# Optimization experiments

Measured on AMD Instinct MI355X. Metric: run time of the kernel, lower is better.

## Reference

```python
import jax, jax.numpy as jnp
import numpy as np

S = 14
L_COORD = 5.0
L_NOOBJ = 0.5


def setup_inputs() -> dict:
    key = jax.random.key(0)
    k1, k2, k3, k4 = jax.random.split(key, 4)
    N = 4096
    # positive uniforms so sqrt(w), sqrt(h) and IoU areas are well-defined (as in real YOLO outputs)
    pred_tensor = jax.random.uniform(k1, (N, S, S, 30), dtype=jnp.float32, minval=0.01, maxval=1.0)
    target_boxes = jax.random.uniform(k2, (N, S, S, 4), dtype=jnp.float32, minval=0.01, maxval=1.0)
    target_cls = jax.random.uniform(k3, (N, S, S, 20), dtype=jnp.float32)
    has_object_map = jax.random.bernoulli(k4, 0.15, (N, S, S))
    return {"pred_tensor": pred_tensor, "target_boxes": target_boxes,
            "target_cls": target_cls, "has_object_map": has_object_map}


def _xywh2xyxy(b):
    # b: (..., 4) as [cx, cy, w, h]; cx,cy are in grid units -> divide by S
    x, y, w, h = b[..., 0], b[..., 1], b[..., 2], b[..., 3]
    return jnp.stack([x / S - 0.5 * w, y / S - 0.5 * h,
                      x / S + 0.5 * w, y / S + 0.5 * h], axis=-1)


def _iou_pairwise(b1, b2):
    # elementwise IoU between matched boxes (diag of compute_iou), b: (..., 4) xyxy
    lt = jnp.maximum(b1[..., :2], b2[..., :2])
    rb = jnp.minimum(b1[..., 2:], b2[..., 2:])
    wh = jnp.maximum(rb - lt, 0.0)
    inter = wh[..., 0] * wh[..., 1]
    a1 = (b1[..., 2] - b1[..., 0]) * (b1[..., 3] - b1[..., 1])
    a2 = (b2[..., 2] - b2[..., 0]) * (b2[..., 3] - b2[..., 1])
    return inter / (a1 + a2 - inter)


def reference(pred_tensor, target_boxes, target_cls, has_object_map):
    N = pred_tensor.shape[0]
    obj = has_object_map.astype(pred_tensor.dtype)          # (N,S,S)
    noobj = 1.0 - obj

    box1 = pred_tensor[..., 0:5]
    box2 = pred_tensor[..., 5:10]
    pred_cls = pred_tensor[..., 10:]

    # class loss: masked sum-MSE over object cells
    cls_loss = jnp.sum(obj[..., None] * (pred_cls - target_cls) ** 2)

    # no-object loss: confidences of both predictors in non-object cells vs 0
    no_obj_loss = L_NOOBJ * jnp.sum(noobj * (box1[..., 4] ** 2 + box2[..., 4] ** 2))

    # best-of-B selection by IoU against target (elementwise, matched per cell)
    tgt_xyxy = _xywh2xyxy(target_boxes)
    iou1 = _iou_pairwise(_xywh2xyxy(box1[..., :4]), tgt_xyxy)
    iou2 = _iou_pairwise(_xywh2xyxy(box2[..., :4]), tgt_xyxy)
    take1 = iou1 > iou2
    best_iou = jnp.where(take1, iou1, iou2)                  # (N,S,S)
    best_box = jnp.where(take1[..., None], box1, box2)       # (N,S,S,5)

    xy_err = jnp.sum((best_box[..., :2] - target_boxes[..., :2]) ** 2, axis=-1)
    wh_err = jnp.sum((jnp.sqrt(best_box[..., 2:4]) - jnp.sqrt(target_boxes[..., 2:4])) ** 2, axis=-1)
    reg_loss = L_COORD * jnp.sum(obj * (xy_err + wh_err))

    # containing-object confidence loss; target IoU is detached
    contain_loss = jnp.sum(obj * (best_box[..., 4] - jax.lax.stop_gradient(best_iou)) ** 2)

    total = cls_loss + no_obj_loss + contain_loss + reg_loss
    # [total, reg, containing_obj, no_obj, cls], each averaged over batch
    return jnp.stack([total, reg_loss, contain_loss, no_obj_loss, cls_loss]) / N
```

## Files before the change

kernel.cpp:

```cpp
#include <hip/hip_runtime.h>


#define CELLS   802816
#define THREADS 256
#define NBLK    1024
#define NWAVES  (NBLK * 4)
#define CHUNK   32
#define CHUNKS  (CELLS / CHUNK)
#define L_COORD 5.0f
#define L_NOOBJ 0.5f

__global__ __launch_bounds__(THREADS, 4) void yolo_main(
    const float* __restrict__ pred,
    const float* __restrict__ tbox,
    const float* __restrict__ tcls,
    const int*   __restrict__ objmap,
    float4*      __restrict__ part)
{
    __shared__ float lds[4 * 960];
    __shared__ float red[4][4];

    const int tid  = threadIdx.x;
    const int wv   = tid >> 6;
    const int lane = tid & 63;
    float*  seg = &lds[wv * 960];
    float4* s4  = (float4*)seg;

    const int cc0 = lane / 5,   ch0 = (lane - cc0 * 5) * 4;
    const int i1  = lane + 64;
    const int cc1 = i1 / 5,     ch1 = (i1 - cc1 * 5) * 4;
    const int i2  = lane + 128;
    const int cc2 = (lane < 32) ? (i2 / 5) : 0;
    const int ch2 = (lane < 32) ? (i2 - cc2 * 5) * 4 : 0;
    const int bcell = lane >> 1;
    const int box   = lane & 1;
    const float invS = 1.0f / 14.0f;

    float acc_reg = 0.f, acc_cont = 0.f, acc_noobj = 0.f, acc_cls = 0.f;

    int c = blockIdx.x * 4 + wv;

    {
        const float4* p4 = (const float4*)pred + (size_t)c * 240;
        const float4* t4 = (const float4*)tcls + (size_t)c * 160;
        const int*    ob = objmap + (size_t)c * CHUNK;
        float4 v0 = p4[lane], v1 = p4[i1], v2 = p4[i2], v3;
        if (lane < 48) v3 = p4[lane + 192];
        float4 t0 = t4[lane], t1 = t4[i1], t2;
        if (lane < 32) t2 = t4[i2];
        float4 tb = ((const float4*)tbox)[(size_t)c * CHUNK + bcell];
        int o0 = ob[cc0], o1 = ob[cc1], o2 = ob[cc2], ox = ob[bcell];

        s4[lane] = v0; s4[i1] = v1; s4[i2] = v2;
        if (lane < 48) s4[lane + 192] = v3;

        for (;;) {
            const int  cn = c + NWAVES;
            const bool hn = cn < CHUNKS;

            float4 nv0, nv1, nv2, nv3, nt0, nt1, nt2, ntb;
            int no0 = 0, no1 = 0, no2 = 0, nox = 0;
            if (hn) {
                const float4* np4 = (const float4*)pred + (size_t)cn * 240;
                const float4* nt4 = (const float4*)tcls + (size_t)cn * 160;
                const int*    nob = objmap + (size_t)cn * CHUNK;
                nv0 = np4[lane]; nv1 = np4[i1]; nv2 = np4[i2];
                if (lane < 48) nv3 = np4[lane + 192];
                nt0 = nt4[lane]; nt1 = nt4[i1];
                if (lane < 32) nt2 = nt4[i2];
                ntb = ((const float4*)tbox)[(size_t)cn * CHUNK + bcell];
                no0 = nob[cc0]; no1 = nob[cc1]; no2 = nob[cc2]; nox = nob[bcell];
            }

            {
                float cl = 0.f;
                if (o0) {
                    const float2 a = *(const float2*)&seg[cc0 * 30 + 10 + ch0];
                    const float2 b = *(const float2*)&seg[cc0 * 30 + 12 + ch0];
                    float d0 = a.x - t0.x, d1 = a.y - t0.y;
                    float d2 = b.x - t0.z, d3 = b.y - t0.w;
                    cl += d0*d0 + d1*d1 + d2*d2 + d3*d3;
                }
                if (o1) {
                    const float2 a = *(const float2*)&seg[cc1 * 30 + 10 + ch1];
                    const float2 b = *(const float2*)&seg[cc1 * 30 + 12 + ch1];
                    float d0 = a.x - t1.x, d1 = a.y - t1.y;
                    float d2 = b.x - t1.z, d3 = b.y - t1.w;
                    cl += d0*d0 + d1*d1 + d2*d2 + d3*d3;
                }
                if ((lane < 32) && o2) {
                    const float2 a = *(const float2*)&seg[cc2 * 30 + 10 + ch2];
                    const float2 b = *(const float2*)&seg[cc2 * 30 + 12 + ch2];
                    float d0 = a.x - t2.x, d1 = a.y - t2.y;
                    float d2 = b.x - t2.z, d3 = b.y - t2.w;
                    cl += d0*d0 + d1*d1 + d2*d2 + d3*d3;
                }
                acc_cls += cl;
            }
            {
                const float* pp = &seg[bcell * 30 + box * 5];
                float x = pp[0], y = pp[1], w = pp[2], h = pp[3], conf = pp[4];
                if (!ox) acc_noobj += conf * conf;

                float txc = tb.x * invS, tyc = tb.y * invS;
                float tx1 = txc - 0.5f * tb.z, ty1 = tyc - 0.5f * tb.w;
                float tx2 = txc + 0.5f * tb.z, ty2 = tyc + 0.5f * tb.w;
                float ta  = (tx2 - tx1) * (ty2 - ty1);

                float ax1 = x * invS - 0.5f * w, ay1 = y * invS - 0.5f * h;
                float ax2 = x * invS + 0.5f * w, ay2 = y * invS + 0.5f * h;
                float a1  = (ax2 - ax1) * (ay2 - ay1);
                float iw  = fmaxf(fminf(ax2, tx2) - fmaxf(ax1, tx1), 0.f);
                float ih  = fmaxf(fminf(ay2, ty2) - fmaxf(ay1, ty1), 0.f);
                float inter = iw * ih;
                float iou   = inter / (a1 + ta - inter);

                float iou_o = __shfl_xor(iou, 1);
                bool win = (box == 0) ? (iou > iou_o) : !(iou_o > iou);
                if (win && ox) {
                    float dx = x - tb.x, dy = y - tb.y;
                    float dw = sqrtf(w) - sqrtf(tb.z);
                    float dh = sqrtf(h) - sqrtf(tb.w);
                    acc_reg  += dx*dx + dy*dy + dw*dw + dh*dh;
                    float dc  = conf - iou;
                    acc_cont += dc * dc;
                }
            }

            if (!hn) break;

            s4[lane] = nv0; s4[i1] = nv1; s4[i2] = nv2;
            if (lane < 48) s4[lane + 192] = nv3;
            t0 = nt0; t1 = nt1; t2 = nt2; tb = ntb;
            o0 = no0; o1 = no1; o2 = no2; ox = nox;
            c = cn;
        }
    }

    #pragma unroll
    for (int off = 32; off > 0; off >>= 1) {
        acc_reg   += __shfl_down(acc_reg,   off);
        acc_cont  += __shfl_down(acc_cont,  off);
        acc_noobj += __shfl_down(acc_noobj, off);
        acc_cls   += __shfl_down(acc_cls,   off);
    }
    if (lane == 0) {
        red[wv][0] = acc_reg;
        red[wv][1] = acc_cont;
        red[wv][2] = acc_noobj;
        red[wv][3] = acc_cls;
    }
    __syncthreads();
    if (tid == 0) {
        float4 p;
        p.x = red[0][0] + red[1][0] + red[2][0] + red[3][0];
        p.y = red[0][1] + red[1][1] + red[2][1] + red[3][1];
        p.z = red[0][2] + red[1][2] + red[2][2] + red[3][2];
        p.w = red[0][3] + red[1][3] + red[2][3] + red[3][3];
        part[blockIdx.x] = p;
    }
}

__global__ __launch_bounds__(1024) void yolo_reduce(
    const float4* __restrict__ part, float* __restrict__ out)
{
    __shared__ float red[16][4];
    float r = 0.f, c = 0.f, n = 0.f, cl = 0.f;
    for (int i = threadIdx.x; i < NBLK; i += 1024) {
        float4 p = part[i];
        r += p.x; c += p.y; n += p.z; cl += p.w;
    }
    #pragma unroll
    for (int off = 32; off > 0; off >>= 1) {
        r  += __shfl_down(r,  off);
        c  += __shfl_down(c,  off);
        n  += __shfl_down(n,  off);
        cl += __shfl_down(cl, off);
    }
    const int wave = threadIdx.x >> 6, lane = threadIdx.x & 63;
    if (lane == 0) {
        red[wave][0] = r; red[wave][1] = c; red[wave][2] = n; red[wave][3] = cl;
    }
    __syncthreads();
    if (threadIdx.x == 0) {
        float R = 0.f, C = 0.f, Nn = 0.f, Cl = 0.f;
        #pragma unroll
        for (int w = 0; w < 16; ++w) {
            R += red[w][0]; C += red[w][1]; Nn += red[w][2]; Cl += red[w][3];
        }
        const float invN = 1.0f / 4096.0f;
        float reg   = L_COORD * R  * invN;
        float cont  =           C  * invN;
        float noobj = L_NOOBJ * Nn * invN;
        float cls   =           Cl * invN;
        out[0] = reg + cont + noobj + cls;
        out[1] = reg;
        out[2] = cont;
        out[3] = noobj;
        out[4] = cls;
    }
}

extern "C" void kernel_launch(void* const* d_in, const int* in_sizes, int n_in,
                              void* d_out, int out_size, void* d_ws, size_t ws_size,
                              hipStream_t stream) {
    const float* pred   = (const float*)d_in[0];
    const float* tbox   = (const float*)d_in[1];
    const float* tcls   = (const float*)d_in[2];
    const int*   objmap = (const int*)  d_in[3];
    float4* part = (float4*)d_ws;
    float*  out  = (float*)d_out;

    yolo_main<<<NBLK, THREADS, 0, stream>>>(pred, tbox, tcls, objmap, part);
    yolo_reduce<<<1, 1024, 0, stream>>>(part, out);
}
```

Measured before the change: 202.0 us.

## Prefetch object masks upfront, fully unroll chunk loop, and redirect masked loads

```diff
diff --git a/kernel.cpp b/kernel.cpp
--- a/kernel.cpp
+++ b/kernel.cpp
@@ -7,8 +7,88 @@
 #define NWAVES  (NBLK * 4)
 #define CHUNK   32
 #define CHUNKS  (CELLS / CHUNK)
+#define MAXSLOT 7
 #define L_COORD 5.0f
 #define L_NOOBJ 0.5f
+
+#define ISSUE(cn, opk, P, T, Bx) do {                                         \
+    const float4* t4_ = (const float4*)tcls + (size_t)(cn) * 160;             \
+    const float4* p4_ = (const float4*)pred + (size_t)(cn) * 240;             \
+    T[0] = t4_[((opk) & 1) ? lane : 0];                                       \
+    T[1] = t4_[((opk) & 2) ? i1 : 0];                                         \
+    if (lane < 32) T[2] = t4_[((opk) & 4) ? i2 : 0];                          \
+    Bx = ((const float4*)tbox)[(size_t)(cn) * CHUNK + (((opk) & 8) ? bcell : 0)]; \
+    P[0] = p4_[lane]; P[1] = p4_[i1]; P[2] = p4_[i2];                         \
+    if (lane < 48) P[3] = p4_[lane + 192];                                    \
+  } while (0)
+
+#define STAGE(P) do {                                                         \
+    s4[lane] = P[0]; s4[i1] = P[1]; s4[i2] = P[2];                            \
+    if (lane < 48) s4[lane + 192] = P[3];                                     \
+  } while (0)
+
+#define COMPUTE(opk, T, Bx) do {                                              \
+    float cl_ = 0.f;                                                          \
+    if ((opk) & 1) {                                                          \
+      const float2 a_ = *(const float2*)&seg[cc0 * 30 + 10 + ch0];            \
+      const float2 b_ = *(const float2*)&seg[cc0 * 30 + 12 + ch0];            \
+      float d0_ = a_.x - T[0].x, d1_ = a_.y - T[0].y;                         \
+      float d2_ = b_.x - T[0].z, d3_ = b_.y - T[0].w;                         \
+      cl_ += d0_*d0_ + d1_*d1_ + d2_*d2_ + d3_*d3_;                           \
+    }                                                                         \
+    if ((opk) & 2) {                                                          \
+      const float2 a_ = *(const float2*)&seg[cc1 * 30 + 10 + ch1];            \
+      const float2 b_ = *(const float2*)&seg[cc1 * 30 + 12 + ch1];            \
+      float d0_ = a_.x - T[1].x, d1_ = a_.y - T[1].y;                         \
+      float d2_ = b_.x - T[1].z, d3_ = b_.y - T[1].w;                         \
+      cl_ += d0_*d0_ + d1_*d1_ + d2_*d2_ + d3_*d3_;                           \
+    }                                                                         \
+    if ((lane < 32) && ((opk) & 4)) {                                         \
+      const float2 a_ = *(const float2*)&seg[cc2 * 30 + 10 + ch2];            \
+      const float2 b_ = *(const float2*)&seg[cc2 * 30 + 12 + ch2];            \
+      float d0_ = a_.x - T[2].x, d1_ = a_.y - T[2].y;                         \
+      float d2_ = b_.x - T[2].z, d3_ = b_.y - T[2].w;                         \
+      cl_ += d0_*d0_ + d1_*d1_ + d2_*d2_ + d3_*d3_;                           \
+    }                                                                         \
+    acc_cls += cl_;                                                           \
+    const float* pp_ = &seg[bcell * 30 + box * 5];                            \
+    float x_ = pp_[0], y_ = pp_[1], w_ = pp_[2], h_ = pp_[3], cf_ = pp_[4];   \
+    const bool ox_ = ((opk) & 8) != 0;                                        \
+    if (!ox_) acc_noobj += cf_ * cf_;                                         \
+    float txc_ = Bx.x * invS, tyc_ = Bx.y * invS;                             \
+    float tx1_ = txc_ - 0.5f * Bx.z, ty1_ = tyc_ - 0.5f * Bx.w;               \
+    float tx2_ = txc_ + 0.5f * Bx.z, ty2_ = tyc_ + 0.5f * Bx.w;               \
+    float ta_  = (tx2_ - tx1_) * (ty2_ - ty1_);                               \
+    float ax1_ = x_ * invS - 0.5f * w_, ay1_ = y_ * invS - 0.5f * h_;         \
+    float ax2_ = x_ * invS + 0.5f * w_, ay2_ = y_ * invS + 0.5f * h_;         \
+    float a1_  = (ax2_ - ax1_) * (ay2_ - ay1_);                               \
+    float iw_  = fmaxf(fminf(ax2_, tx2_) - fmaxf(ax1_, tx1_), 0.f);           \
+    float ih_  = fmaxf(fminf(ay2_, ty2_) - fmaxf(ay1_, ty1_), 0.f);           \
+    float in_  = iw_ * ih_;                                                   \
+    float iou_ = in_ / (a1_ + ta_ - in_);                                     \
+    float iouo_ = __shfl_xor(iou_, 1);                                        \
+    bool win_ = (box == 0) ? (iou_ > iouo_) : !(iouo_ > iou_);                \
+    if (win_ && ox_) {                                                        \
+      float dx_ = x_ - Bx.x, dy_ = y_ - Bx.y;                                 \
+      float dw_ = sqrtf(w_) - sqrtf(Bx.z);                                    \
+      float dh_ = sqrtf(h_) - sqrtf(Bx.w);                                    \
+      acc_reg  += dx_*dx_ + dy_*dy_ + dw_*dw_ + dh_*dh_;                      \
+      float dc_ = cf_ - iou_;                                                 \
+      acc_cont += dc_ * dc_;                                                  \
+    }                                                                         \
+  } while (0)
+
+#define SLOT(s, PX, TX, BX, PY, TY, BY) do {                                  \
+    const int c_ = w0 + (s) * NWAVES;                                         \
+    if (c_ < CHUNKS) {                                                        \
+      STAGE(PX);                                                              \
+      __builtin_amdgcn_sched_barrier(0);                                      \
+      const int cn_ = c_ + NWAVES;                                            \
+      if (cn_ < CHUNKS) ISSUE(cn_, opack[(s) + 1], PY, TY, BY);               \
+      __builtin_amdgcn_sched_barrier(0);                                      \
+      COMPUTE(opack[(s)], TX, BX);                                            \
+    }                                                                         \
+  } while (0)
 
 __global__ __launch_bounds__(THREADS, 4) void yolo_main(
     const float* __restrict__ pred,
@@ -38,104 +118,37 @@
 
     float acc_reg = 0.f, acc_cont = 0.f, acc_noobj = 0.f, acc_cls = 0.f;
 
-    int c = blockIdx.x * 4 + wv;
-
-    {
-        const float4* p4 = (const float4*)pred + (size_t)c * 240;
-        const float4* t4 = (const float4*)tcls + (size_t)c * 160;
-        const int*    ob = objmap + (size_t)c * CHUNK;
-        float4 v0 = p4[lane], v1 = p4[i1], v2 = p4[i2], v3;
-        if (lane < 48) v3 = p4[lane + 192];
-        float4 t0 = t4[lane], t1 = t4[i1], t2;
-        if (lane < 32) t2 = t4[i2];
-        float4 tb = ((const float4*)tbox)[(size_t)c * CHUNK + bcell];
-        int o0 = ob[cc0], o1 = ob[cc1], o2 = ob[cc2], ox = ob[bcell];
-
-        s4[lane] = v0; s4[i1] = v1; s4[i2] = v2;
-        if (lane < 48) s4[lane + 192] = v3;
-
-        for (;;) {
-            const int  cn = c + NWAVES;
-            const bool hn = cn < CHUNKS;
-
-            float4 nv0, nv1, nv2, nv3, nt0, nt1, nt2, ntb;
-            int no0 = 0, no1 = 0, no2 = 0, nox = 0;
-            if (hn) {
-                const float4* np4 = (const float4*)pred + (size_t)cn * 240;
-                const float4* nt4 = (const float4*)tcls + (size_t)cn * 160;
-                const int*    nob = objmap + (size_t)cn * CHUNK;
-                nv0 = np4[lane]; nv1 = np4[i1]; nv2 = np4[i2];
-                if (lane < 48) nv3 = np4[lane + 192];
-                nt0 = nt4[lane]; nt1 = nt4[i1];
-                if (lane < 32) nt2 = nt4[i2];
-                ntb = ((const float4*)tbox)[(size_t)cn * CHUNK + bcell];
-                no0 = nob[cc0]; no1 = nob[cc1]; no2 = nob[cc2]; nox = nob[bcell];
-            }
-
-            {
-                float cl = 0.f;
-                if (o0) {
-                    const float2 a = *(const float2*)&seg[cc0 * 30 + 10 + ch0];
-                    const float2 b = *(const float2*)&seg[cc0 * 30 + 12 + ch0];
-                    float d0 = a.x - t0.x, d1 = a.y - t0.y;
-                    float d2 = b.x - t0.z, d3 = b.y - t0.w;
-                    cl += d0*d0 + d1*d1 + d2*d2 + d3*d3;
-                }
-                if (o1) {
-                    const float2 a = *(const float2*)&seg[cc1 * 30 + 10 + ch1];
-                    const float2 b = *(const float2*)&seg[cc1 * 30 + 12 + ch1];
-                    float d0 = a.x - t1.x, d1 = a.y - t1.y;
-                    float d2 = b.x - t1.z, d3 = b.y - t1.w;
-                    cl += d0*d0 + d1*d1 + d2*d2 + d3*d3;
-                }
-                if ((lane < 32) && o2) {
-                    const float2 a = *(const float2*)&seg[cc2 * 30 + 10 + ch2];
-                    const float2 b = *(const float2*)&seg[cc2 * 30 + 12 + ch2];
-                    float d0 = a.x - t2.x, d1 = a.y - t2.y;
-                    float d2 = b.x - t2.z, d3 = b.y - t2.w;
-                    cl += d0*d0 + d1*d1 + d2*d2 + d3*d3;
-                }
-                acc_cls += cl;
-            }
-            {
-                const float* pp = &seg[bcell * 30 + box * 5];
-                float x = pp[0], y = pp[1], w = pp[2], h = pp[3], conf = pp[4];
-                if (!ox) acc_noobj += conf * conf;
-
-                float txc = tb.x * invS, tyc = tb.y * invS;
-                float tx1 = txc - 0.5f * tb.z, ty1 = tyc - 0.5f * tb.w;
-                float tx2 = txc + 0.5f * tb.z, ty2 = tyc + 0.5f * tb.w;
-                float ta  = (tx2 - tx1) * (ty2 - ty1);
-
-                float ax1 = x * invS - 0.5f * w, ay1 = y * invS - 0.5f * h;
-                float ax2 = x * invS + 0.5f * w, ay2 = y * invS + 0.5f * h;
-                float a1  = (ax2 - ax1) * (ay2 - ay1);
-                float iw  = fmaxf(fminf(ax2, tx2) - fmaxf(ax1, tx1), 0.f);
-                float ih  = fmaxf(fminf(ay2, ty2) - fmaxf(ay1, ty1), 0.f);
-                float inter = iw * ih;
-                float iou   = inter / (a1 + ta - inter);
-
-                float iou_o = __shfl_xor(iou, 1);
-                bool win = (box == 0) ? (iou > iou_o) : !(iou_o > iou);
-                if (win && ox) {
-                    float dx = x - tb.x, dy = y - tb.y;
-                    float dw = sqrtf(w) - sqrtf(tb.z);
-                    float dh = sqrtf(h) - sqrtf(tb.w);
-                    acc_reg  += dx*dx + dy*dy + dw*dw + dh*dh;
-                    float dc  = conf - iou;
-                    acc_cont += dc * dc;
-                }
-            }
-
-            if (!hn) break;
-
-            s4[lane] = nv0; s4[i1] = nv1; s4[i2] = nv2;
-            if (lane < 48) s4[lane + 192] = nv3;
-            t0 = nt0; t1 = nt1; t2 = nt2; tb = ntb;
-            o0 = no0; o1 = no1; o2 = no2; ox = nox;
-            c = cn;
+    const int w0 = blockIdx.x * 4 + wv;
+
+    int opack[MAXSLOT + 1];
+    #pragma unroll
+    for (int s = 0; s < MAXSLOT; ++s) {
+        const int c = w0 + s * NWAVES;
+        int v = 0;
+        if (c < CHUNKS) {
+            const int* ob = objmap + (size_t)c * CHUNK;
+            v  = ob[cc0]  ? 1 : 0;
+            v |= ob[cc1]  ? 2 : 0;
+            v |= ob[cc2]  ? 4 : 0;
+            v |= ob[bcell]? 8 : 0;
         }
-    }
+        opack[s] = v;
+    }
+    opack[MAXSLOT] = 0;
+
+    float4 PA[4], TA[3], BA;
+    float4 PB[4], TB[3], BB;
+
+    ISSUE(w0, opack[0], PA, TA, BA);
+    __builtin_amdgcn_sched_barrier(0);
+
+    SLOT(0, PA, TA, BA, PB, TB, BB);
+    SLOT(1, PB, TB, BB, PA, TA, BA);
+    SLOT(2, PA, TA, BA, PB, TB, BB);
+    SLOT(3, PB, TB, BB, PA, TA, BA);
+    SLOT(4, PA, TA, BA, PB, TB, BB);
+    SLOT(5, PB, TB, BB, PA, TA, BA);
+    SLOT(6, PA, TA, BA, PB, TB, BB);
 
     #pragma unroll
     for (int off = 32; off > 0; off >>= 1) {
```

Result: slower. 214.1 us (+6.0%).
